# Kernel optimization log

Hardware: AMD Instinct MI355X
Metric: run time of the kernel (lower is better)

The kernel has to match this reference:

```python
import jax, jax.numpy as jnp
from jax import lax
import numpy as np

B, TIN, F, H, TOUT = 256, 512, 64, 512, 64


def setup_inputs() -> dict:
    key = jax.random.key(0)
    ks = jax.random.split(key, 16)
    s = 0.05

    def p(k, shape):
        return jax.random.normal(k, shape, jnp.float32) * s

    inp = {
        "x": jax.random.normal(ks[0], (B, TIN, F), jnp.float32),
        "y": jax.random.normal(ks[1], (B, TOUT), jnp.float32),
    }
    i = 2
    for name, insz in [("enc0", F), ("enc1", H), ("dec0", 1), ("dec1", H)]:
        inp[name + "_Wih"] = p(ks[i], (4 * H, insz)); i += 1
        inp[name + "_Whh"] = p(ks[i], (4 * H, H)); i += 1
        inp[name + "_bih"] = jnp.zeros((4 * H,), jnp.float32)
        inp[name + "_bhh"] = jnp.zeros((4 * H,), jnp.float32)
    inp["proj_W"] = p(ks[i], (1, H)); i += 1
    inp["proj_b"] = jnp.zeros((1,), jnp.float32)
    return inp


def _cell(xt, h, c, Wih, Whh, bih, bhh):
    # PyTorch gate order: i, f, g, o
    g = xt @ Wih.T + h @ Whh.T + bih + bhh  # [B, 4H]
    i, f, gg, o = jnp.split(g, 4, axis=-1)
    c = jax.nn.sigmoid(f) * c + jax.nn.sigmoid(i) * jnp.tanh(gg)
    h = jax.nn.sigmoid(o) * jnp.tanh(c)
    return h, c


def reference(x, y,
              enc0_Wih, enc0_Whh, enc0_bih, enc0_bhh,
              enc1_Wih, enc1_Whh, enc1_bih, enc1_bhh,
              dec0_Wih, dec0_Whh, dec0_bih, dec0_bhh,
              dec1_Wih, dec1_Whh, dec1_bih, dec1_bhh,
              proj_W, proj_b):
    Bsz = x.shape[0]
    Hd = enc0_Whh.shape[1]
    Tout = y.shape[1]
    z = jnp.zeros((Bsz, Hd), x.dtype)

    def enc_step(carry, xt):
        h0, c0, h1, c1 = carry
        h0, c0 = _cell(xt, h0, c0, enc0_Wih, enc0_Whh, enc0_bih, enc0_bhh)
        h1, c1 = _cell(h0, h1, c1, enc1_Wih, enc1_Whh, enc1_bih, enc1_bhh)
        return (h0, c0, h1, c1), None

    (h0, c0, h1, c1), _ = lax.scan(enc_step, (z, z, z, z), jnp.swapaxes(x, 0, 1))

    prev = x[:, -1, -1:]  # [B, 1]

    def dec_step(carry, _):
        h0, c0, h1, c1, prev = carry
        h0, c0 = _cell(prev, h0, c0, dec0_Wih, dec0_Whh, dec0_bih, dec0_bhh)
        h1, c1 = _cell(h0, h1, c1, dec1_Wih, dec1_Whh, dec1_bih, dec1_bhh)
        step = h1 @ proj_W.T + proj_b  # [B, 1]
        # teacher_forcing = 0.0 -> always feed model prediction back
        return (h0, c0, h1, c1, step), step[:, 0]

    _, outs = lax.scan(dec_step, (h0, c0, h1, c1, prev), None, length=Tout)
    return outs.T  # [B, Tout]
```

## Files before the change

kernel.cpp:

```cpp
#include <hip/hip_runtime.h>

#define TINN 512
#define FF 64
#define HHD 512
#define TOUTN 64

using v8h = __attribute__((ext_vector_type(8))) _Float16;
using v4h = __attribute__((ext_vector_type(4))) _Float16;
using v4f = __attribute__((ext_vector_type(4))) float;
using u32x4 = __attribute__((ext_vector_type(4))) unsigned int;
using u64 = unsigned long long;

#define AGT __HIP_MEMORY_SCOPE_AGENT

#define WOFF 0
#define BIAS_OFF 131072
#define WIH0_OFF 131328
#define PREV_OFF 131584
#define PART_OFF 131840
#define PROJW_OFF 132864
#define PROJB_OFF 134912
#define TRANS_OFF 134976
#define SMEM_TOTAL 137024

#define WS_BAR 0
#define WS_HOFF 16384
#define HBYTES (256 * HHD * 2)
#define WS_XS (WS_HOFF + 6 * HBYTES)
#define XS_TBYTES 32768
#define WS_NEED (WS_XS + (size_t)TINN * XS_TBYTES)

static __device__ __forceinline__ float sigm(float x) { return 1.0f / (1.0f + __expf(-x)); }
static __device__ __forceinline__ float tanh_f(float x) { return 1.0f - 2.0f / (1.0f + __expf(2.0f * x)); }

static __device__ __forceinline__ v8h aload16(const _Float16* p) {
  union { u64 u[2]; v8h h; } c;
  const u64* q = (const u64*)p;
  c.u[0] = __hip_atomic_load(q, __ATOMIC_RELAXED, AGT);
  c.u[1] = __hip_atomic_load(q + 1, __ATOMIC_RELAXED, AGT);
  return c.h;
}
static __device__ __forceinline__ void astore8(_Float16* p, v4h v) {
  union { u64 u; v4h h; } c;
  c.h = v;
  __hip_atomic_store((u64*)p, c.u, __ATOMIC_RELAXED, AGT);
}
static __device__ __forceinline__ void astore8z(void* p) {
  __hip_atomic_store((u64*)p, 0ull, __ATOMIC_RELAXED, AGT);
}

#if __has_builtin(__builtin_amdgcn_raw_ptr_buffer_load_b128) && \
    __has_builtin(__builtin_amdgcn_make_buffer_rsrc)
#define HAVE_BUFLOAD 1
using rsrc_t = __amdgpu_buffer_rsrc_t;
static __device__ __forceinline__ rsrc_t mkrsrc(const void* p) {
  return __builtin_amdgcn_make_buffer_rsrc((void*)p, (short)0, 0xFFFFFFFFu, 0x00020000);
}
static __device__ __forceinline__ v8h bload16(rsrc_t r, int byteOff) {
  union { u32x4 u; v8h h; } c;
  c.u = __builtin_amdgcn_raw_ptr_buffer_load_b128(r, byteOff, 0, 17);
  return c.h;
}
#endif

static __device__ __forceinline__ void signalDone(unsigned* slots, int mySlot, unsigned val) {
  __builtin_amdgcn_s_waitcnt(0);
  __syncthreads();
  if (threadIdx.x == 0)
    __hip_atomic_store(&slots[(size_t)mySlot * 16], val, __ATOMIC_RELAXED, AGT);
}

static __device__ __forceinline__ void waitRole(unsigned* slots, int base, int tgt) {
  if (tgt > 0) {
    if (threadIdx.x < 32) {
      while ((int)__hip_atomic_load(&slots[(size_t)(base + threadIdx.x) * 16],
                                    __ATOMIC_RELAXED, AGT) < tgt)
        __builtin_amdgcn_s_sleep(1);
    }
    __syncthreads();
#if __has_builtin(__builtin_amdgcn_sched_barrier)
    __builtin_amdgcn_sched_barrier(0);
#endif
  }
}

static __device__ __attribute__((noinline)) void loadWeights(
    int tid, int hc0, const float* W1, int ld1, int K1,
    const float* W2, int K) {
  extern __shared__ char smem[];
  int c = tid >> 2, sub = tid & 3;
  int nt = c >> 4, l = c & 15;
  int n = nt * HHD + hc0 + l;
  int Kq = K >> 2;
  for (int k = sub * Kq; k < (sub + 1) * Kq; ++k) {
    float v;
    if (k < K1) v = W1[(size_t)n * ld1 + k];
    else        v = W2[(size_t)n * HHD + (k - K1)];
    int kc = k >> 6, ks = (k >> 5) & 1, quad = (k >> 3) & 3, j = k & 7;
    int off = (((kc * 2 + ks) * 4 + nt) * 64 + quad * 16 + l) * 16 + j * 2;
    *(_Float16*)(smem + WOFF + off) = (_Float16)v;
  }
}

template <int WC0>
static __device__ __forceinline__ void mfma8(
    const _Float16* src, int rt, int lane, const char* wbLane, v4f* acc) {
#if HAVE_BUFLOAD
  rsrc_t rs = mkrsrc(src);
#endif
#pragma unroll
  for (int kc = 0; kc < 8; ++kc) {
    int off = rt * 16384 + kc * 2048 + lane * 16;
    v8h ak0, ak1;
#if HAVE_BUFLOAD
    ak0 = bload16(rs, off);
    ak1 = bload16(rs, off + 1024);
#else
    ak0 = aload16(src + off / 2);
    ak1 = aload16(src + (off + 1024) / 2);
#endif
    const char* bb = wbLane + (size_t)(WC0 + kc) * 8192;
#pragma unroll
    for (int ks = 0; ks < 2; ++ks) {
      v8h a = ks ? ak1 : ak0;
      acc[0] = __builtin_amdgcn_mfma_f32_16x16x32_f16(a, *(const v8h*)(bb + (ks * 4 + 0) * 1024), acc[0], 0, 0, 0);
      acc[1] = __builtin_amdgcn_mfma_f32_16x16x32_f16(a, *(const v8h*)(bb + (ks * 4 + 1) * 1024), acc[1], 0, 0, 0);
      acc[2] = __builtin_amdgcn_mfma_f32_16x16x32_f16(a, *(const v8h*)(bb + (ks * 4 + 2) * 1024), acc[2], 0, 0, 0);
      acc[3] = __builtin_amdgcn_mfma_f32_16x16x32_f16(a, *(const v8h*)(bb + (ks * 4 + 3) * 1024), acc[3], 0, 0, 0);
    }
  }
}

static __device__ __forceinline__ void xChunk(
    const char* xsT, const float* xstep, int m0, int tid,
    const char* wbLane, v4f* acc) {
  int lane = tid & 63, wave = tid >> 6;
  int l15 = lane & 15, quad = lane >> 4;
  v8h ak0, ak1;
  if (xsT != nullptr) {
    int rt = (m0 >> 4) + wave;
    const char* xb = xsT + rt * 2048 + lane * 16;
    ak0 = *(const v8h*)(xb);
    ak1 = *(const v8h*)(xb + 1024);
  } else {
    int ra = m0 + wave * 16 + l15;
    const float* xr = xstep + (size_t)ra * (TINN * FF) + quad * 8;
    v4f f00 = *(const v4f*)(xr);
    v4f f01 = *(const v4f*)(xr + 4);
    v4f f10 = *(const v4f*)(xr + 32);
    v4f f11 = *(const v4f*)(xr + 36);
#pragma unroll
    for (int e = 0; e < 4; ++e) {
      ak0[e] = (_Float16)f00[e]; ak0[4 + e] = (_Float16)f01[e];
      ak1[e] = (_Float16)f10[e]; ak1[4 + e] = (_Float16)f11[e];
    }
  }
#pragma unroll
  for (int ks = 0; ks < 2; ++ks) {
    v8h a = ks ? ak1 : ak0;
    acc[0] = __builtin_amdgcn_mfma_f32_16x16x32_f16(a, *(const v8h*)(wbLane + (ks * 4 + 0) * 1024), acc[0], 0, 0, 0);
    acc[1] = __builtin_amdgcn_mfma_f32_16x16x32_f16(a, *(const v8h*)(wbLane + (ks * 4 + 1) * 1024), acc[1], 0, 0, 0);
    acc[2] = __builtin_amdgcn_mfma_f32_16x16x32_f16(a, *(const v8h*)(wbLane + (ks * 4 + 2) * 1024), acc[2], 0, 0, 0);
    acc[3] = __builtin_amdgcn_mfma_f32_16x16x32_f16(a, *(const v8h*)(wbLane + (ks * 4 + 3) * 1024), acc[3], 0, 0, 0);
  }
}

static __device__ __forceinline__ void epilogue(
    int tid, int m0, int hc0, int rank1, _Float16* hout, float* creg, v4f* acc) {
  extern __shared__ char smem[];
  int lane = tid & 63, wave = tid >> 6;
  int l15 = lane & 15, quad = lane >> 4;
  float* bias = (float*)(smem + BIAS_OFF);
  float bi = bias[l15], bf = bias[16 + l15], bg = bias[32 + l15], bo = bias[48 + l15];
  float wi = 0.f, wf = 0.f, wg = 0.f, wo = 0.f;
  if (rank1) {
    float* wih0 = (float*)(smem + WIH0_OFF);
    wi = wih0[l15]; wf = wih0[16 + l15]; wg = wih0[32 + l15]; wo = wih0[48 + l15];
  }
  float* prevl = (float*)(smem + PREV_OFF);
  _Float16* tb = (_Float16*)(smem + TRANS_OFF + (size_t)wave * 512);
#pragma unroll
  for (int r = 0; r < 4; ++r) {
    int mloc = wave * 16 + quad * 4 + r;
    float gi = acc[0][r] + bi, gf = acc[1][r] + bf;
    float gg = acc[2][r] + bg, go = acc[3][r] + bo;
    if (rank1) {
      float pv = prevl[mloc];
      gi += pv * wi; gf += pv * wf; gg += pv * wg; go += pv * wo;
    }
    float cc = sigm(gf) * creg[r] + sigm(gi) * tanh_f(gg);
    float h = sigm(go) * tanh_f(cc);
    creg[r] = cc;
    tb[(quad * 4 + r) * 16 + l15] = (_Float16)h;
  }
  {
    int mloc = lane & 15, cg = lane >> 4;
    v4h hv = *(const v4h*)(tb + mloc * 16 + cg * 4);
    int m = m0 + wave * 16 + mloc;
    int c0 = hc0 + cg * 4;
    int off = (m >> 4) * 16384 + (c0 >> 6) * 2048 + ((c0 >> 5) & 1) * 1024 +
              ((c0 >> 3) & 3) * 256 + (m & 15) * 16 + (c0 & 7) * 2;
    astore8((_Float16*)((char*)hout + off), hv);
  }
}


static __device__ __attribute__((noinline)) void stepEnc0(
    int tid, int m0, int hc0, unsigned* slots, int mySlot, int p,
    const char* xsT, const float* xstep,
    const _Float16* h0prev, _Float16* h0out, float* creg) {
  extern __shared__ char smem[];
  int lane = tid & 63, wave = tid >> 6;
  v4f acc[4];
  acc[0] = v4f{0.f, 0.f, 0.f, 0.f}; acc[1] = acc[0]; acc[2] = acc[0]; acc[3] = acc[0];
  const char* wbLane = smem + WOFF + (size_t)lane * 16;
  waitRole(slots, 0, p + 1);
  xChunk(xsT, xstep, m0, tid, wbLane, acc);
  mfma8<1>(h0prev, (m0 >> 4) + wave, lane, wbLane, acc);
  waitRole(slots, 32, p - 2);
  epilogue(tid, m0, hc0, 0, h0out, creg, acc);
  signalDone(slots, mySlot, p + 2);
}

static __device__ __attribute__((noinline)) void stepL1(
    int tid, int m0, int hc0, unsigned* slots, int mySlot, int tR1, int tR0,
    const _Float16* h0src, const _Float16* h1prev, _Float16* h1out, float* creg) {
  extern __shared__ char smem[];
  int lane = tid & 63, wave = tid >> 6;
  v4f acc[4];
  acc[0] = v4f{0.f, 0.f, 0.f, 0.f}; acc[1] = acc[0]; acc[2] = acc[0]; acc[3] = acc[0];
  const char* wbLane = smem + WOFF + (size_t)lane * 16;
  int rt = (m0 >> 4) + wave;
  waitRole(slots, 32, tR1);
  mfma8<8>(h1prev, rt, lane, wbLane, acc);
  waitRole(slots, 0, tR0);
  mfma8<0>(h0src, rt, lane, wbLane, acc);
  epilogue(tid, m0, hc0, 0, h1out, creg, acc);
  signalDone(slots, mySlot, tR0);
}

static __device__ __attribute__((noinline)) void stepDec0(
    int tid, int m0, int hc0, unsigned* slots, int mySlot, int u,
    const _Float16* h0prev, _Float16* h0out, float* creg) {
  extern __shared__ char smem[];
  int lane = tid & 63, wave = tid >> 6;
  v4f acc[4];
  acc[0] = v4f{0.f, 0.f, 0.f, 0.f}; acc[1] = acc[0]; acc[2] = acc[0]; acc[3] = acc[0];
  const char* wbLane = smem + WOFF + (size_t)lane * 16;
  waitRole(slots, 0, u + 1);
  mfma8<0>(h0prev, (m0 >> 4) + wave, lane, wbLane, acc);
  epilogue(tid, m0, hc0, 1, h0out, creg, acc);
  signalDone(slots, mySlot, u + 2);
}

__global__ void __launch_bounds__(256, 1)
seq2seq_kernel(const float* x,
               const float* e0wi, const float* e0wh, const float* e0bi, const float* e0bh,
               const float* e1wi, const float* e1wh, const float* e1bi, const float* e1bh,
               const float* d0wi, const float* d0wh, const float* d0bi, const float* d0bh,
               const float* d1wi, const float* d1wh, const float* d1bi, const float* d1bh,
               const float* pw, const float* pb,
               float* out, char* ws, int useXs) {
  extern __shared__ char smem[];
  int tid = threadIdx.x, bid = blockIdx.x;
  int group = bid >> 6;
  int r = bid & 63;
  bool isL1 = (r >= 32);
  int hcTile = r & 31;
  int hc0 = hcTile * 16;
  int m0 = group * 64;
  unsigned* slots = (unsigned*)(ws + WS_BAR) + (size_t)group * 1024;
  int mySlot = isL1 ? 32 + hcTile : hcTile;
  char* xs = useXs ? (ws + WS_XS) : nullptr;

  _Float16* h0b[4]; _Float16* h1b[2];
  h0b[0] = (_Float16*)(ws + WS_HOFF);
  h0b[1] = (_Float16*)(ws + WS_HOFF + 1 * HBYTES);
  h0b[2] = (_Float16*)(ws + WS_HOFF + 2 * HBYTES);
  h0b[3] = (_Float16*)(ws + WS_HOFF + 3 * HBYTES);
  h1b[0] = (_Float16*)(ws + WS_HOFF + 4 * HBYTES);
  h1b[1] = (_Float16*)(ws + WS_HOFF + 5 * HBYTES);

  float creg[4];
  creg[0] = 0.f; creg[1] = 0.f; creg[2] = 0.f; creg[3] = 0.f;

  {
    int t16 = r * 256 + tid;
    char* base = (t16 < 8192) ? (char*)h0b[3] : (char*)h1b[1];
    int idx = t16 & 8191;
    astore8z(base + (size_t)m0 * HHD * 2 + (size_t)idx * 8);
  }

  if (xs) {
    int m = m0 + (tid & 63);
    int cb = (tid >> 6) * 16;
    int rt = m >> 4, l15m = m & 15;
    for (int k = 0; k < 8; ++k) {
      int t = r + k * 64;
      const float* xp = x + (size_t)m * (TINN * FF) + (size_t)t * FF + cb;
      v4f f0 = *(const v4f*)(xp);
      v4f f1 = *(const v4f*)(xp + 4);
      v4f f2 = *(const v4f*)(xp + 8);
      v4f f3 = *(const v4f*)(xp + 12);
      v4h h0_, h1_, h2_, h3_;
#pragma unroll
      for (int e = 0; e < 4; ++e) {
        h0_[e] = (_Float16)f0[e]; h1_[e] = (_Float16)f1[e];
        h2_[e] = (_Float16)f2[e]; h3_[e] = (_Float16)f3[e];
      }
      char* xt = xs + (size_t)t * XS_TBYTES;
      v4h hs[4] = {h0_, h1_, h2_, h3_};
#pragma unroll
      for (int s = 0; s < 4; ++s) {
        int c0 = cb + 4 * s;
        int off = (rt * 2 + ((c0 >> 5) & 1)) * 1024 +
                  ((c0 >> 3) & 3) * 256 + l15m * 16 + (c0 & 7) * 2;
        astore8((_Float16*)(xt + off), hs[s]);
      }
    }
  }

  if (!isL1) {
    loadWeights(tid, hc0, e0wi, 64, 64, e0wh, 576);
    if (tid < 64) {
      int n = (tid >> 4) * HHD + hc0 + (tid & 15);
      ((float*)(smem + BIAS_OFF))[tid] = e0bi[n] + e0bh[n];
    }
  } else {
    loadWeights(tid, hc0, e1wi, 512, 512, e1wh, 1024);
    if (tid < 64) {
      int n = (tid >> 4) * HHD + hc0 + (tid & 15);
      ((float*)(smem + BIAS_OFF))[tid] = e1bi[n] + e1bh[n];
    }
  }
  signalDone(slots, mySlot, 1);

  if (!isL1) {
    for (int p = 0; p < TINN; ++p)
      stepEnc0(tid, m0, hc0, slots, mySlot, p,
               xs ? xs + (size_t)p * XS_TBYTES : nullptr,
               xs ? nullptr : x + (size_t)p * FF,
               h0b[(p + 3) & 3], h0b[p & 3], creg);
    loadWeights(tid, hc0, d0wh, 512, 512, nullptr, 512);
    if (tid < 64) {
      int n = (tid >> 4) * HHD + hc0 + (tid & 15);
      ((float*)(smem + BIAS_OFF))[tid] = d0bi[n] + d0bh[n];
      ((float*)(smem + WIH0_OFF))[tid] = d0wi[n];
    }
    for (int k = tid; k < 512; k += 256) ((float*)(smem + PROJW_OFF))[k] = pw[k];
    if (tid == 0) ((float*)(smem + PROJB_OFF))[0] = pb[0];
    for (int t = 0; t <= TOUTN; ++t) {
      int u = TINN + t;
      waitRole(slots, 32, u + 1);
      float* prevl = (float*)(smem + PREV_OFF);
      if (t == 0) {
        if (tid < 64)
          prevl[tid] = x[(size_t)(m0 + tid) * (TINN * FF) + 511 * 64 + 63];
      } else {
        float* part = (float*)(smem + PART_OFF);
        float* pjw = (float*)(smem + PROJW_OFF);
        const _Float16* h1base = h1b[(u + 1) & 1];
        int m = m0 + (tid >> 2);
        int rt = m >> 4, l15m = m & 15;
        int kc0 = (tid & 3) * 2;
        float s = 0.f;
#pragma unroll
        for (int kc = kc0; kc < kc0 + 2; ++kc)
#pragma unroll
          for (int ks = 0; ks < 2; ++ks)
#pragma unroll
            for (int q = 0; q < 4; ++q) {
              int off = (rt * 8 + kc) * 2048 + ks * 1024 + q * 256 + l15m * 16;
              v8h hv = aload16(h1base + off / 2);
              const float* w = pjw + kc * 64 + ks * 32 + q * 8;
#pragma unroll
              for (int e = 0; e < 8; ++e) s += (float)hv[e] * w[e];
            }
        part[tid] = s;
        __syncthreads();
        if (tid < 64) {
          float p4 = part[tid * 4] + part[tid * 4 + 1] + part[tid * 4 + 2] +
                     part[tid * 4 + 3] + ((float*)(smem + PROJB_OFF))[0];
          prevl[tid] = p4;
          if (hcTile == 0) out[(size_t)(m0 + tid) * TOUTN + (t - 1)] = p4;
        }
      }
      __syncthreads();
      if (t < TOUTN)
        stepDec0(tid, m0, hc0, slots, mySlot, u, h0b[(u + 3) & 3], h0b[u & 3], creg);
    }
  } else {
    for (int s = 0; s < TINN; ++s)
      stepL1(tid, m0, hc0, slots, mySlot, s + 1, s + 2,
             h0b[s & 3], h1b[(s + 1) & 1], h1b[s & 1], creg);
    loadWeights(tid, hc0, d1wi, 512, 512, d1wh, 1024);
    if (tid < 64) {
      int n = (tid >> 4) * HHD + hc0 + (tid & 15);
      ((float*)(smem + BIAS_OFF))[tid] = d1bi[n] + d1bh[n];
    }
    for (int t = 0; t < TOUTN; ++t) {
      int u = TINN + t;
      stepL1(tid, m0, hc0, slots, mySlot, u + 1, u + 2,
             h0b[u & 3], h1b[(u + 1) & 1], h1b[u & 1], creg);
    }
  }
}

extern "C" void kernel_launch(void* const* d_in, const int* in_sizes, int n_in,
                              void* d_out, int out_size, void* d_ws, size_t ws_size,
                              hipStream_t stream) {
  const float* x = (const float*)d_in[0];
  const float* e0wi = (const float*)d_in[2];
  const float* e0wh = (const float*)d_in[3];
  const float* e0bi = (const float*)d_in[4];
  const float* e0bh = (const float*)d_in[5];
  const float* e1wi = (const float*)d_in[6];
  const float* e1wh = (const float*)d_in[7];
  const float* e1bi = (const float*)d_in[8];
  const float* e1bh = (const float*)d_in[9];
  const float* d0wi = (const float*)d_in[10];
  const float* d0wh = (const float*)d_in[11];
  const float* d0bi = (const float*)d_in[12];
  const float* d0bh = (const float*)d_in[13];
  const float* d1wi = (const float*)d_in[14];
  const float* d1wh = (const float*)d_in[15];
  const float* d1bi = (const float*)d_in[16];
  const float* d1bh = (const float*)d_in[17];
  const float* pw = (const float*)d_in[18];
  const float* pb = (const float*)d_in[19];

  int useXs = (ws_size >= WS_NEED) ? 1 : 0;
  (void)hipFuncSetAttribute((const void*)seq2seq_kernel,
                            hipFuncAttributeMaxDynamicSharedMemorySize, SMEM_TOTAL);
  (void)hipMemsetAsync(d_ws, 0, 16384, stream);
  seq2seq_kernel<<<dim3(256), dim3(256), SMEM_TOTAL, stream>>>(
      x, e0wi, e0wh, e0bi, e0bh, e1wi, e1wh, e1bi, e1bh,
      d0wi, d0wh, d0bi, d0bh, d1wi, d1wh, d1bi, d1bh,
      pw, pb, (float*)d_out, (char*)d_ws, useXs);
}
```

Baseline: 4.564 ms.

## Merge role waits into one combined spin and batch both hidden-state loads

Adds a waitRoles helper that polls both producer slot groups (layer-0 and layer-1 blocks) in a single spin followed by one barrier, instead of two sequential waits. Encoder layer 0 now computes the x-projection before waiting, then waits on both dependencies at once. Layer 1 waits for both inputs up front and uses mfmaDual, which issues all 32 global loads of h1 and h0 before running the MFMAs, so load latency overlaps. This removes one barrier per step and puts more loads in flight. The cost is higher VGPR pressure from 32 v8h registers, and layer 1 can no longer start its h1 MFMAs before h0 is ready.

```diff
diff --git a/kernel.cpp b/kernel.cpp
--- a/kernel.cpp
+++ b/kernel.cpp
@@ -82,6 +82,22 @@
     __builtin_amdgcn_sched_barrier(0);
 #endif
   }
+}
+
+static __device__ __forceinline__ void waitRoles(unsigned* slots, int tgt0, int tgt1) {
+  int t = threadIdx.x;
+  if (t < 64) {
+    int tgt = (t < 32) ? tgt0 : tgt1;
+    if (tgt > 0) {
+      unsigned* p = &slots[(size_t)t * 16];
+      while ((int)__hip_atomic_load(p, __ATOMIC_RELAXED, AGT) < tgt)
+        __builtin_amdgcn_s_sleep(1);
+    }
+  }
+  __syncthreads();
+#if __has_builtin(__builtin_amdgcn_sched_barrier)
+  __builtin_amdgcn_sched_barrier(0);
+#endif
 }
 
 static __device__ __attribute__((noinline)) void loadWeights(
@@ -123,6 +139,65 @@
 #pragma unroll
     for (int ks = 0; ks < 2; ++ks) {
       v8h a = ks ? ak1 : ak0;
+      acc[0] = __builtin_amdgcn_mfma_f32_16x16x32_f16(a, *(const v8h*)(bb + (ks * 4 + 0) * 1024), acc[0], 0, 0, 0);
+      acc[1] = __builtin_amdgcn_mfma_f32_16x16x32_f16(a, *(const v8h*)(bb + (ks * 4 + 1) * 1024), acc[1], 0, 0, 0);
+      acc[2] = __builtin_amdgcn_mfma_f32_16x16x32_f16(a, *(const v8h*)(bb + (ks * 4 + 2) * 1024), acc[2], 0, 0, 0);
+      acc[3] = __builtin_amdgcn_mfma_f32_16x16x32_f16(a, *(const v8h*)(bb + (ks * 4 + 3) * 1024), acc[3], 0, 0, 0);
+    }
+  }
+}
+
+static __device__ __forceinline__ void mfmaDual(
+    const _Float16* h0src, const _Float16* h1src, int rt, int lane,
+    const char* wbLane, v4f* acc) {
+  v8h a1[16], a0[16];
+#if HAVE_BUFLOAD
+  rsrc_t r1 = mkrsrc(h1src);
+  rsrc_t r0 = mkrsrc(h0src);
+#pragma unroll
+  for (int kc = 0; kc < 8; ++kc) {
+    int off = rt * 16384 + kc * 2048 + lane * 16;
+    a1[2 * kc]     = bload16(r1, off);
+    a1[2 * kc + 1] = bload16(r1, off + 1024);
+  }
+#pragma unroll
+  for (int kc = 0; kc < 8; ++kc) {
+    int off = rt * 16384 + kc * 2048 + lane * 16;
+    a0[2 * kc]     = bload16(r0, off);
+    a0[2 * kc + 1] = bload16(r0, off + 1024);
+  }
+#else
+#pragma unroll
+  for (int kc = 0; kc < 8; ++kc) {
+    int off = rt * 16384 + kc * 2048 + lane * 16;
+    a1[2 * kc]     = aload16(h1src + off / 2);
+    a1[2 * kc + 1] = aload16(h1src + (off + 1024) / 2);
+  }
+#pragma unroll
+  for (int kc = 0; kc < 8; ++kc) {
+    int off = rt * 16384 + kc * 2048 + lane * 16;
+    a0[2 * kc]     = aload16(h0src + off / 2);
+    a0[2 * kc + 1] = aload16(h0src + (off + 1024) / 2);
+  }
+#endif
+#pragma unroll
+  for (int kc = 0; kc < 8; ++kc) {
+    const char* bb = wbLane + (size_t)(8 + kc) * 8192;
+#pragma unroll
+    for (int ks = 0; ks < 2; ++ks) {
+      v8h a = a1[2 * kc + ks];
+      acc[0] = __builtin_amdgcn_mfma_f32_16x16x32_f16(a, *(const v8h*)(bb + (ks * 4 + 0) * 1024), acc[0], 0, 0, 0);
+      acc[1] = __builtin_amdgcn_mfma_f32_16x16x32_f16(a, *(const v8h*)(bb + (ks * 4 + 1) * 1024), acc[1], 0, 0, 0);
+      acc[2] = __builtin_amdgcn_mfma_f32_16x16x32_f16(a, *(const v8h*)(bb + (ks * 4 + 2) * 1024), acc[2], 0, 0, 0);
+      acc[3] = __builtin_amdgcn_mfma_f32_16x16x32_f16(a, *(const v8h*)(bb + (ks * 4 + 3) * 1024), acc[3], 0, 0, 0);
+    }
+  }
+#pragma unroll
+  for (int kc = 0; kc < 8; ++kc) {
+    const char* bb = wbLane + (size_t)kc * 8192;
+#pragma unroll
+    for (int ks = 0; ks < 2; ++ks) {
+      v8h a = a0[2 * kc + ks];
       acc[0] = __builtin_amdgcn_mfma_f32_16x16x32_f16(a, *(const v8h*)(bb + (ks * 4 + 0) * 1024), acc[0], 0, 0, 0);
       acc[1] = __builtin_amdgcn_mfma_f32_16x16x32_f16(a, *(const v8h*)(bb + (ks * 4 + 1) * 1024), acc[1], 0, 0, 0);
       acc[2] = __builtin_amdgcn_mfma_f32_16x16x32_f16(a, *(const v8h*)(bb + (ks * 4 + 2) * 1024), acc[2], 0, 0, 0);
@@ -214,10 +289,14 @@
   v4f acc[4];
   acc[0] = v4f{0.f, 0.f, 0.f, 0.f}; acc[1] = acc[0]; acc[2] = acc[0]; acc[3] = acc[0];
   const char* wbLane = smem + WOFF + (size_t)lane * 16;
-  waitRole(slots, 0, p + 1);
-  xChunk(xsT, xstep, m0, tid, wbLane, acc);
+  if (p == 0) {
+    waitRoles(slots, 1, 0);
+    xChunk(xsT, xstep, m0, tid, wbLane, acc);
+  } else {
+    xChunk(xsT, xstep, m0, tid, wbLane, acc);
+    waitRoles(slots, p + 1, p - 2);
+  }
   mfma8<1>(h0prev, (m0 >> 4) + wave, lane, wbLane, acc);
-  waitRole(slots, 32, p - 2);
   epilogue(tid, m0, hc0, 0, h0out, creg, acc);
   signalDone(slots, mySlot, p + 2);
 }
@@ -231,10 +310,8 @@
   acc[0] = v4f{0.f, 0.f, 0.f, 0.f}; acc[1] = acc[0]; acc[2] = acc[0]; acc[3] = acc[0];
   const char* wbLane = smem + WOFF + (size_t)lane * 16;
   int rt = (m0 >> 4) + wave;
-  waitRole(slots, 32, tR1);
-  mfma8<8>(h1prev, rt, lane, wbLane, acc);
-  waitRole(slots, 0, tR0);
-  mfma8<0>(h0src, rt, lane, wbLane, acc);
+  waitRoles(slots, tR0, tR1);
+  mfmaDual(h0src, h1prev, rt, lane, wbLane, acc);
   epilogue(tid, m0, hc0, 0, h1out, creg, acc);
   signalDone(slots, mySlot, tR0);
 }
```

Result: no change. 4.478 ms (-1.9%).
